# Kernel optimization log

Measured on AMD Instinct MI355X. Metric: run time of the kernel, lower is better.

The kernel has to match this reference:

```python
import jax, jax.numpy as jnp
import numpy as np

R = 3            # window radius -> (2R+1)^2 = 49 neighbors
N = 128          # grid side, n
K = 131          # 3 + 64 + 64 channels
C = 21           # num_classes
B = 2            # batch
W = (2 * R + 1) ** 2


def setup_inputs() -> dict:
    key = jax.random.key(0)
    k1, k2, k3, k4 = jax.random.split(key, 4)
    return {
        "intergrated": jax.random.normal(k1, (B, K, N, N), jnp.float32),
        "x2": jax.random.normal(k2, (B, C, N * N), jnp.float32),
        "sel_mask": jax.random.randint(k3, (B, N, N), 0, 2).astype(jnp.int32),
        "conv_parameter": jax.random.uniform(k4, (K,), jnp.float32),
    }


def _shifts(x, r):
    """Gather (2r+1)^2 shifted copies: x [..., n, n] -> [..., n, n, W].
    Entry w=(di,dj) holds x[i+di-r, j+dj-r] (zero-padded out of bounds)."""
    n = x.shape[-1]
    pad = [(0, 0)] * (x.ndim - 2) + [(r, r), (r, r)]
    xp = jnp.pad(x, pad)
    cols = [xp[..., di:di + n, dj:dj + n]
            for di in range(2 * r + 1) for dj in range(2 * r + 1)]
    return jnp.stack(cols, axis=-1)


def _rwn_single(feats, x2b, maskb, conv_parameter):
    """feats [K,n,n], x2b [C,n^2], maskb [n,n] int -> y [n^2, C]."""
    n = feats.shape[-1]
    m = maskb.astype(feats.dtype)            # sampled-pixel indicator
    xm = feats * m                            # sparse-sampled features [K,n,n]
    nbr = _shifts(xm, R)                      # [K,n,n,W] neighbor values
    valid = _shifts(jnp.ones((n, n), feats.dtype), R) > 0  # [n,n,W] in-bounds
    # per-channel windowed L1 distance, exp, per-pixel normalization (softmax
    # of +distance over the valid window, as in the original code)
    d = jnp.abs(xm[..., None] - nbr)          # [K,n,n,W]
    e = jnp.where(valid[None], jnp.exp(d), 0.0)
    a = e / e.sum(axis=-1, keepdims=True)     # rows sum to 1 per channel
    # W = sum_k conv_parameter[k] * a_k, rows only for selected pixels
    A = jnp.einsum('k,kijw->ijw', conv_parameter, a) * m[..., None]  # [n,n,W]
    # y[q,c] = sum_p W[p,q] * x2[p,c]  (W^T @ x2^T, per original col/row swap)
    feat = x2b.reshape(C, n, n)
    msg = A[None] * feat[..., None]           # [C,n,n,W]
    ypad = jnp.zeros((C, n + 2 * R, n + 2 * R), feats.dtype)
    w = 0
    for di in range(2 * R + 1):
        for dj in range(2 * R + 1):
            ypad = ypad.at[:, di:di + n, dj:dj + n].add(msg[..., w])
            w += 1
    y = ypad[:, R:R + n, R:R + n].reshape(C, n * n)
    return y.T                                 # [n^2, C]


def reference(intergrated, x2, sel_mask, conv_parameter):
    f = lambda fe, xb, mb: _rwn_single(fe, xb, mb, conv_parameter)
    return jax.vmap(f)(intergrated, x2, sel_mask)  # [B, n^2, C]
```

## Files before the change

### kernel.cpp

```cpp
#include <hip/hip_runtime.h>

#define R_ 3
#define D_ 7
#define W_ 49
#define N_ 128
#define K_ 131
#define C_ 21
#define B_ 2
#define NN (N_ * N_)
#define TI_ 8
#define TJ_ 16
#define PROWS (TI_ + 2 * R_)
#define PCOLS (TJ_ + 2 * R_)
#define PSTR 24
#define NELEM (PROWS * PCOLS)
#define LDSP (PROWS * PSTR + 8)
#define KC 8
#define KCHUNK ((K_ + KC - 1) / KC)
#define NTAP 28

__global__ __launch_bounds__(256) void rwn_affinity(
    const float* __restrict__ feats,
    const int*   __restrict__ mask,
    const float* __restrict__ cp,
    float* __restrict__ Aout)
{
    __shared__ float2 patch2[LDSP];

    const int tile = blockIdx.x;
    const int kc   = blockIdx.y;
    const int b    = blockIdx.z;
    const int tr = tile >> 3, tc = tile & 7;
    const int ti0 = tr * TI_, tj0 = tc * TJ_;

    const int tid = threadIdx.x;
    const int pix = tid >> 1;
    const int h   = tid & 1;
    const int ti = pix >> 4;
    const int tj = pix & 15;
    const int gi = ti0 + ti, gj = tj0 + tj;

    int   soff[2];
    float swt[2];
    float ozw[2];
    int   slds[2];
    #pragma unroll
    for (int r = 0; r < 2; ++r) {
        int e = tid + r * 256;
        bool act = (e < NELEM);
        int pr = e / PCOLS, pc = e - pr * PCOLS;
        int mi = ti0 + pr - R_, mj = tj0 + pc - R_;
        bool inb = act && mi >= 0 && mi < N_ && mj >= 0 && mj < N_;
        int cmi = mi < 0 ? 0 : (mi > N_ - 1 ? N_ - 1 : mi);
        int cmj = mj < 0 ? 0 : (mj > N_ - 1 ? N_ - 1 : mj);
        soff[r] = cmi * N_ + cmj;
        swt[r]  = inb ? (float)mask[b * NN + soff[r]] : 0.f;
        ozw[r]  = inb ? 1.f : 0.f;
        slds[r] = act ? (pr * PSTR + pc) : (PROWS * PSTR + 4);
    }

    const float ph = h ? 0.f : 1.f;
    const int cbase = ti * PSTR + tj;
    const int bh = cbase + h;

    float Aacc[NTAP];
    #pragma unroll
    for (int i = 0; i < NTAP; ++i) Aacc[i] = 0.f;

    const int k0 = kc * KCHUNK;
    const int k1 = (k0 + KCHUNK < K_) ? (k0 + KCHUNK) : K_;
    const float* fb = feats + (size_t)b * K_ * NN;

    for (int e = tid; e < LDSP; e += 256) patch2[e] = make_float2(0.f, 0.f);

    const float* fk0 = fb + (size_t)k0 * NN;
    float pre0 = fk0[soff[0]] * swt[0];
    float pre1 = fk0[soff[1]] * swt[1];

    __syncthreads();

    for (int k = k0; k < k1; ++k) {
        patch2[slds[0]] = make_float2(ozw[0] * __expf(pre0), ozw[0] * __expf(-pre0));
        patch2[slds[1]] = make_float2(ozw[1] * __expf(pre1), ozw[1] * __expf(-pre1));
        float n0 = 0.f, n1 = 0.f;
        if (k + 1 < k1) {
            const float* fn = fb + (size_t)(k + 1) * NN;
            n0 = fn[soff[0]] * swt[0];
            n1 = fn[soff[1]] * swt[1];
        }
        __syncthreads();

        const float2 cpair = patch2[cbase + R_ * PSTR + R_];
        float ex[NTAP];
        float dsum = 0.f;
        #pragma unroll
        for (int u = 0; u < D_; ++u) {
            #pragma unroll
            for (int s = 0; s < 4; ++s) {
                const int idx = u * 4 + s;
                const float2 np = patch2[bh + u * PSTR + 2 * s];
                float t = fmaxf(cpair.x * np.y, np.x * cpair.y);
                if (s == 3) t *= ph;
                ex[idx] = t;
                dsum += t;
            }
        }
        const float denom = dsum + __shfl_xor(dsum, 1, 64);
        const float scale = cp[k] * __frcp_rn(denom);
        #pragma unroll
        for (int idx = 0; idx < NTAP; ++idx) Aacc[idx] += scale * ex[idx];
        __syncthreads();

        pre0 = n0; pre1 = n1;
    }

    if (mask[b * NN + gi * N_ + gj] != 0) {
        const int pixg = gi * N_ + gj;
        float* ab = Aout + (size_t)b * W_ * NN + h * NN + pixg;
        #pragma unroll
        for (int u = 0; u < D_; ++u) {
            #pragma unroll
            for (int s = 0; s < 4; ++s) {
                if (h == 0 || s < 3)
                    atomicAdd(ab + (u * D_ + 2 * s) * NN, Aacc[u * 4 + s]);
            }
        }
    }
}

#define RSTR 25
__global__ __launch_bounds__(256) void rwn_gather(
    const float* __restrict__ Aarr,
    const float* __restrict__ x2,
    float* __restrict__ out)
{
    __shared__ float red[4 * 64 * RSTR];

    const int q0 = blockIdx.x * 64;
    const int b  = blockIdx.y;
    const int tid = threadIdx.x;
    const int qh = tid & 63;
    const int wg = tid >> 6;
    const int q = q0 + qh;
    const int i = q >> 7, j = q & (N_ - 1);

    const float* Ab = Aarr + (size_t)b * W_ * NN;
    const float* xb = x2 + (size_t)b * C_ * NN;

    float acc[C_];
    #pragma unroll
    for (int c = 0; c < C_; ++c) acc[c] = 0.f;

    #pragma unroll
    for (int rep = 0; rep < 2; ++rep) {
        const int uu = wg + rep * 4;
        if (uu > 6) break;
        const int pi = i - (uu - R_);
        const int cpi = pi < 0 ? 0 : (pi > N_ - 1 ? N_ - 1 : pi);
        const float rv = (pi >= 0 && pi < N_) ? 1.f : 0.f;
        const float* Aw = Ab + (size_t)uu * D_ * NN;
        #pragma unroll
        for (int v = 0; v < D_; ++v) {
            const int pj = j - (v - R_);
            const int cpj = pj < 0 ? 0 : (pj > N_ - 1 ? N_ - 1 : pj);
            const float vv = (pj >= 0 && pj < N_) ? rv : 0.f;
            const int p = cpi * N_ + cpj;
            const float a = vv * Aw[(size_t)v * NN + p];
            #pragma unroll
            for (int c = 0; c < C_; ++c)
                acc[c] += a * xb[(size_t)c * NN + p];
        }
    }

    float* rbase = red + (wg * 64 + qh) * RSTR;
    #pragma unroll
    for (int c = 0; c < C_; ++c) rbase[c] = acc[c];
    __syncthreads();

    float* ob = out + ((size_t)b * NN + q0) * C_;
    for (int e = tid; e < 64 * C_; e += 256) {
        const int qq = e / C_, cc = e - qq * C_;
        const int a = qq * RSTR + cc;
        ob[e] = red[a] + red[64 * RSTR + a] + red[128 * RSTR + a] + red[192 * RSTR + a];
    }
}

extern "C" void kernel_launch(void* const* d_in, const int* in_sizes, int n_in,
                              void* d_out, int out_size, void* d_ws, size_t ws_size,
                              hipStream_t stream) {
    const float* feats = (const float*)d_in[0];
    const float* x2    = (const float*)d_in[1];
    const int*   mask  = (const int*)d_in[2];
    const float* cp    = (const float*)d_in[3];
    float* out = (float*)d_out;

    float* Aarr = (float*)d_ws;
    const size_t Abytes = (size_t)B_ * W_ * NN * sizeof(float);

    hipMemsetAsync(Aarr, 0, Abytes, stream);

    dim3 gridA(128, KC, B_);
    rwn_affinity<<<gridA, 256, 0, stream>>>(feats, mask, cp, Aarr);

    dim3 gridG(NN / 64, B_);
    rwn_gather<<<gridG, 256, 0, stream>>>(Aarr, x2, out);
}
```

Measured before the change: 154.2 us.

## Use four threads per pixel and 512-thread blocks in affinity and gather

The affinity kernel now assigns four threads per pixel, each computing one or two full window rows (14 taps instead of 28), with a two-step shuffle reduction for the softmax denominator. The K split drops from 8 to 4 chunks, so there are fewer atomic adds per output element. The gather kernel uses 512 threads, giving one warp group per window row with an 8-way LDS reduction. The aim is more parallelism per pixel, lower register pressure and fewer redundant atomics, at the cost of a longer serial k-loop per block and more shuffle and LDS traffic.

```diff
diff --git a/kernel.cpp b/kernel.cpp
--- a/kernel.cpp
+++ b/kernel.cpp
@@ -14,12 +14,11 @@
 #define PCOLS (TJ_ + 2 * R_)
 #define PSTR 24
 #define NELEM (PROWS * PCOLS)
-#define LDSP (PROWS * PSTR + 8)
-#define KC 8
+#define LDSP ((PROWS + 1) * PSTR)
+#define KC 4
 #define KCHUNK ((K_ + KC - 1) / KC)
-#define NTAP 28
 
-__global__ __launch_bounds__(256) void rwn_affinity(
+__global__ __launch_bounds__(512, 4) void rwn_affinity(
     const float* __restrict__ feats,
     const int*   __restrict__ mask,
     const float* __restrict__ cp,
@@ -34,107 +33,98 @@
     const int ti0 = tr * TI_, tj0 = tc * TJ_;
 
     const int tid = threadIdx.x;
-    const int pix = tid >> 1;
-    const int h   = tid & 1;
+    const int pix = tid >> 2;
+    const int h   = tid & 3;
     const int ti = pix >> 4;
     const int tj = pix & 15;
     const int gi = ti0 + ti, gj = tj0 + tj;
 
-    int   soff[2];
-    float swt[2];
-    float ozw[2];
-    int   slds[2];
+    const bool act = (tid < NELEM);
+    int pr = tid / PCOLS, pc = tid - pr * PCOLS;
+    int mi = ti0 + pr - R_, mj = tj0 + pc - R_;
+    const bool inb = act && mi >= 0 && mi < N_ && mj >= 0 && mj < N_;
+    int cmi = mi < 0 ? 0 : (mi > N_ - 1 ? N_ - 1 : mi);
+    int cmj = mj < 0 ? 0 : (mj > N_ - 1 ? N_ - 1 : mj);
+    const int   soff = inb ? (cmi * N_ + cmj) : 0;
+    const float swt  = inb ? (float)mask[b * NN + soff] : 0.f;
+    const float ozw  = inb ? 1.f : 0.f;
+    const int   slds = pr * PSTR + pc;
+
+    const int cbase = ti * PSTR + tj;
+    const int ub0 = cbase + h * PSTR;
+    const int ub1 = (h < 3) ? (cbase + (h + 4) * PSTR) : (PROWS * PSTR + tj);
+
+    float Aacc[14];
     #pragma unroll
-    for (int r = 0; r < 2; ++r) {
-        int e = tid + r * 256;
-        bool act = (e < NELEM);
-        int pr = e / PCOLS, pc = e - pr * PCOLS;
-        int mi = ti0 + pr - R_, mj = tj0 + pc - R_;
-        bool inb = act && mi >= 0 && mi < N_ && mj >= 0 && mj < N_;
-        int cmi = mi < 0 ? 0 : (mi > N_ - 1 ? N_ - 1 : mi);
-        int cmj = mj < 0 ? 0 : (mj > N_ - 1 ? N_ - 1 : mj);
-        soff[r] = cmi * N_ + cmj;
-        swt[r]  = inb ? (float)mask[b * NN + soff[r]] : 0.f;
-        ozw[r]  = inb ? 1.f : 0.f;
-        slds[r] = act ? (pr * PSTR + pc) : (PROWS * PSTR + 4);
-    }
-
-    const float ph = h ? 0.f : 1.f;
-    const int cbase = ti * PSTR + tj;
-    const int bh = cbase + h;
-
-    float Aacc[NTAP];
-    #pragma unroll
-    for (int i = 0; i < NTAP; ++i) Aacc[i] = 0.f;
+    for (int i = 0; i < 14; ++i) Aacc[i] = 0.f;
 
     const int k0 = kc * KCHUNK;
     const int k1 = (k0 + KCHUNK < K_) ? (k0 + KCHUNK) : K_;
     const float* fb = feats + (size_t)b * K_ * NN;
 
-    for (int e = tid; e < LDSP; e += 256) patch2[e] = make_float2(0.f, 0.f);
+    for (int e = tid; e < PSTR; e += 512)
+        patch2[PROWS * PSTR + e] = make_float2(0.f, 0.f);
 
-    const float* fk0 = fb + (size_t)k0 * NN;
-    float pre0 = fk0[soff[0]] * swt[0];
-    float pre1 = fk0[soff[1]] * swt[1];
+    float pre = fb[(size_t)k0 * NN + soff] * swt;
 
     __syncthreads();
 
     for (int k = k0; k < k1; ++k) {
-        patch2[slds[0]] = make_float2(ozw[0] * __expf(pre0), ozw[0] * __expf(-pre0));
-        patch2[slds[1]] = make_float2(ozw[1] * __expf(pre1), ozw[1] * __expf(-pre1));
-        float n0 = 0.f, n1 = 0.f;
-        if (k + 1 < k1) {
-            const float* fn = fb + (size_t)(k + 1) * NN;
-            n0 = fn[soff[0]] * swt[0];
-            n1 = fn[soff[1]] * swt[1];
-        }
+        if (act)
+            patch2[slds] = make_float2(ozw * __expf(pre), ozw * __expf(-pre));
+        float nx = 0.f;
+        if (k + 1 < k1)
+            nx = fb[(size_t)(k + 1) * NN + soff] * swt;
         __syncthreads();
 
         const float2 cpair = patch2[cbase + R_ * PSTR + R_];
-        float ex[NTAP];
+        float ex[14];
         float dsum = 0.f;
         #pragma unroll
-        for (int u = 0; u < D_; ++u) {
-            #pragma unroll
-            for (int s = 0; s < 4; ++s) {
-                const int idx = u * 4 + s;
-                const float2 np = patch2[bh + u * PSTR + 2 * s];
-                float t = fmaxf(cpair.x * np.y, np.x * cpair.y);
-                if (s == 3) t *= ph;
-                ex[idx] = t;
-                dsum += t;
-            }
+        for (int v = 0; v < D_; ++v) {
+            const float2 np = patch2[ub0 + v];
+            float t = fmaxf(cpair.x * np.y, np.x * cpair.y);
+            ex[v] = t;
+            dsum += t;
         }
-        const float denom = dsum + __shfl_xor(dsum, 1, 64);
-        const float scale = cp[k] * __frcp_rn(denom);
         #pragma unroll
-        for (int idx = 0; idx < NTAP; ++idx) Aacc[idx] += scale * ex[idx];
+        for (int v = 0; v < D_; ++v) {
+            const float2 np = patch2[ub1 + v];
+            float t = fmaxf(cpair.x * np.y, np.x * cpair.y);
+            ex[7 + v] = t;
+            dsum += t;
+        }
+        dsum += __shfl_xor(dsum, 1, 64);
+        dsum += __shfl_xor(dsum, 2, 64);
+        const float scale = cp[k] * __frcp_rn(dsum);
+        #pragma unroll
+        for (int idx = 0; idx < 14; ++idx) Aacc[idx] += scale * ex[idx];
         __syncthreads();
 
-        pre0 = n0; pre1 = n1;
+        pre = nx;
     }
 
     if (mask[b * NN + gi * N_ + gj] != 0) {
         const int pixg = gi * N_ + gj;
-        float* ab = Aout + (size_t)b * W_ * NN + h * NN + pixg;
+        float* ab = Aout + (size_t)b * W_ * NN + pixg;
         #pragma unroll
-        for (int u = 0; u < D_; ++u) {
+        for (int v = 0; v < D_; ++v)
+            atomicAdd(ab + (h * D_ + v) * NN, Aacc[v]);
+        if (h < 3) {
             #pragma unroll
-            for (int s = 0; s < 4; ++s) {
-                if (h == 0 || s < 3)
-                    atomicAdd(ab + (u * D_ + 2 * s) * NN, Aacc[u * 4 + s]);
-            }
+            for (int v = 0; v < D_; ++v)
+                atomicAdd(ab + ((h + 4) * D_ + v) * NN, Aacc[7 + v]);
         }
     }
 }
 
-#define RSTR 25
-__global__ __launch_bounds__(256) void rwn_gather(
+#define RSTR 22
+__global__ __launch_bounds__(512, 4) void rwn_gather(
     const float* __restrict__ Aarr,
     const float* __restrict__ x2,
     float* __restrict__ out)
 {
-    __shared__ float red[4 * 64 * RSTR];
+    __shared__ float red[8 * 64 * RSTR];
 
     const int q0 = blockIdx.x * 64;
     const int b  = blockIdx.y;
@@ -151,14 +141,11 @@
     #pragma unroll
     for (int c = 0; c < C_; ++c) acc[c] = 0.f;
 
-    #pragma unroll
-    for (int rep = 0; rep < 2; ++rep) {
-        const int uu = wg + rep * 4;
-        if (uu > 6) break;
-        const int pi = i - (uu - R_);
+    if (wg < D_) {
+        const int pi = i - (wg - R_);
         const int cpi = pi < 0 ? 0 : (pi > N_ - 1 ? N_ - 1 : pi);
         const float rv = (pi >= 0 && pi < N_) ? 1.f : 0.f;
-        const float* Aw = Ab + (size_t)uu * D_ * NN;
+        const float* Aw = Ab + (size_t)wg * D_ * NN;
         #pragma unroll
         for (int v = 0; v < D_; ++v) {
             const int pj = j - (v - R_);
@@ -178,10 +165,14 @@
     __syncthreads();
 
     float* ob = out + ((size_t)b * NN + q0) * C_;
-    for (int e = tid; e < 64 * C_; e += 256) {
+    for (int e = tid; e < 64 * C_; e += 512) {
         const int qq = e / C_, cc = e - qq * C_;
         const int a = qq * RSTR + cc;
-        ob[e] = red[a] + red[64 * RSTR + a] + red[128 * RSTR + a] + red[192 * RSTR + a];
+        float s = 0.f;
+        #pragma unroll
+        for (int pl = 0; pl < 8; ++pl)
+            s += red[pl * 64 * RSTR + a];
+        ob[e] = s;
     }
 }
 
@@ -200,8 +191,8 @@
     hipMemsetAsync(Aarr, 0, Abytes, stream);
 
     dim3 gridA(128, KC, B_);
-    rwn_affinity<<<gridA, 256, 0, stream>>>(feats, mask, cp, Aarr);
+    rwn_affinity<<<gridA, 512, 0, stream>>>(feats, mask, cp, Aarr);
 
     dim3 gridG(NN / 64, B_);
-    rwn_gather<<<gridG, 256, 0, stream>>>(Aarr, x2, out);
+    rwn_gather<<<gridG, 512, 0, stream>>>(Aarr, x2, out);
 }
```

Measured after the change: 164.9 us. +6.9%, slower.

## Accumulate affinity taps in packed fp16 and widen gather to one row per wave

Applied to the files above, without the earlier changes.

The affinity kernel now packs pairs of window taps into half-precision vectors and does the per-channel scale-and-accumulate with packed fp16 FMAs. This halves the accumulator register count and the FMA instruction count. The exponentials switch to exp2f, with log2(e) folded into the mask weight. The gather kernel goes from 256 to 512 threads so that each of 7 waves handles one window row, and its final reduction sums 8 partial planes. The fp16 accumulation costs accuracy and can overflow when channel distances are large.

```diff
diff --git a/kernel.cpp b/kernel.cpp
--- a/kernel.cpp
+++ b/kernel.cpp
@@ -1,4 +1,5 @@
 #include <hip/hip_runtime.h>
+#include <hip/hip_fp16.h>
 
 #define R_ 3
 #define D_ 7
@@ -17,7 +18,8 @@
 #define LDSP (PROWS * PSTR + 8)
 #define KC 8
 #define KCHUNK ((K_ + KC - 1) / KC)
-#define NTAP 28
+
+typedef __fp16 h2 __attribute__((ext_vector_type(2)));
 
 __global__ __launch_bounds__(256) void rwn_affinity(
     const float* __restrict__ feats,
@@ -40,6 +42,7 @@
     const int tj = pix & 15;
     const int gi = ti0 + ti, gj = tj0 + tj;
 
+    const float LOG2E = 1.4426950408889634f;
     int   soff[2];
     float swt[2];
     float ozw[2];
@@ -54,7 +57,7 @@
         int cmi = mi < 0 ? 0 : (mi > N_ - 1 ? N_ - 1 : mi);
         int cmj = mj < 0 ? 0 : (mj > N_ - 1 ? N_ - 1 : mj);
         soff[r] = cmi * N_ + cmj;
-        swt[r]  = inb ? (float)mask[b * NN + soff[r]] : 0.f;
+        swt[r]  = inb ? ((float)mask[b * NN + soff[r]] * LOG2E) : 0.f;
         ozw[r]  = inb ? 1.f : 0.f;
         slds[r] = act ? (pr * PSTR + pc) : (PROWS * PSTR + 4);
     }
@@ -63,9 +66,9 @@
     const int cbase = ti * PSTR + tj;
     const int bh = cbase + h;
 
-    float Aacc[NTAP];
-    #pragma unroll
-    for (int i = 0; i < NTAP; ++i) Aacc[i] = 0.f;
+    h2 Aacc[14];
+    #pragma unroll
+    for (int i = 0; i < 14; ++i) Aacc[i] = (h2){(__fp16)0.f, (__fp16)0.f};
 
     const int k0 = kc * KCHUNK;
     const int k1 = (k0 + KCHUNK < K_) ? (k0 + KCHUNK) : K_;
@@ -80,8 +83,8 @@
     __syncthreads();
 
     for (int k = k0; k < k1; ++k) {
-        patch2[slds[0]] = make_float2(ozw[0] * __expf(pre0), ozw[0] * __expf(-pre0));
-        patch2[slds[1]] = make_float2(ozw[1] * __expf(pre1), ozw[1] * __expf(-pre1));
+        patch2[slds[0]] = make_float2(ozw[0] * exp2f(pre0), ozw[0] * exp2f(-pre0));
+        patch2[slds[1]] = make_float2(ozw[1] * exp2f(pre1), ozw[1] * exp2f(-pre1));
         float n0 = 0.f, n1 = 0.f;
         if (k + 1 < k1) {
             const float* fn = fb + (size_t)(k + 1) * NN;
@@ -91,24 +94,27 @@
         __syncthreads();
 
         const float2 cpair = patch2[cbase + R_ * PSTR + R_];
-        float ex[NTAP];
+        h2 ex[14];
         float dsum = 0.f;
         #pragma unroll
         for (int u = 0; u < D_; ++u) {
             #pragma unroll
-            for (int s = 0; s < 4; ++s) {
-                const int idx = u * 4 + s;
-                const float2 np = patch2[bh + u * PSTR + 2 * s];
-                float t = fmaxf(cpair.x * np.y, np.x * cpair.y);
-                if (s == 3) t *= ph;
-                ex[idx] = t;
-                dsum += t;
+            for (int m = 0; m < 2; ++m) {
+                const float2 np0 = patch2[bh + u * PSTR + 4 * m];
+                const float2 np1 = patch2[bh + u * PSTR + 4 * m + 2];
+                float t0 = fmaxf(cpair.x * np0.y, np0.x * cpair.y);
+                float t1 = fmaxf(cpair.x * np1.y, np1.x * cpair.y);
+                if (m == 1) t1 *= ph;
+                dsum += t0;
+                dsum += t1;
+                ex[u * 2 + m] = __builtin_amdgcn_cvt_pkrtz(t0, t1);
             }
         }
         const float denom = dsum + __shfl_xor(dsum, 1, 64);
         const float scale = cp[k] * __frcp_rn(denom);
-        #pragma unroll
-        for (int idx = 0; idx < NTAP; ++idx) Aacc[idx] += scale * ex[idx];
+        const h2 s2 = __builtin_amdgcn_cvt_pkrtz(scale, scale);
+        #pragma unroll
+        for (int m = 0; m < 14; ++m) Aacc[m] = ex[m] * s2 + Aacc[m];
         __syncthreads();
 
         pre0 = n0; pre1 = n1;
@@ -120,21 +126,23 @@
         #pragma unroll
         for (int u = 0; u < D_; ++u) {
             #pragma unroll
-            for (int s = 0; s < 4; ++s) {
-                if (h == 0 || s < 3)
-                    atomicAdd(ab + (u * D_ + 2 * s) * NN, Aacc[u * 4 + s]);
+            for (int m = 0; m < 2; ++m) {
+                const h2 tv = Aacc[u * 2 + m];
+                atomicAdd(ab + (u * D_ + 4 * m) * NN, (float)tv[0]);
+                if (h == 0 || m < 1)
+                    atomicAdd(ab + (u * D_ + 4 * m + 2) * NN, (float)tv[1]);
             }
         }
     }
 }
 
-#define RSTR 25
-__global__ __launch_bounds__(256) void rwn_gather(
+#define RSTR 22
+__global__ __launch_bounds__(512, 4) void rwn_gather(
     const float* __restrict__ Aarr,
     const float* __restrict__ x2,
     float* __restrict__ out)
 {
-    __shared__ float red[4 * 64 * RSTR];
+    __shared__ float red[8 * 64 * RSTR];
 
     const int q0 = blockIdx.x * 64;
     const int b  = blockIdx.y;
@@ -151,14 +159,11 @@
     #pragma unroll
     for (int c = 0; c < C_; ++c) acc[c] = 0.f;
 
-    #pragma unroll
-    for (int rep = 0; rep < 2; ++rep) {
-        const int uu = wg + rep * 4;
-        if (uu > 6) break;
-        const int pi = i - (uu - R_);
+    if (wg < D_) {
+        const int pi = i - (wg - R_);
         const int cpi = pi < 0 ? 0 : (pi > N_ - 1 ? N_ - 1 : pi);
         const float rv = (pi >= 0 && pi < N_) ? 1.f : 0.f;
-        const float* Aw = Ab + (size_t)uu * D_ * NN;
+        const float* Aw = Ab + (size_t)wg * D_ * NN;
         #pragma unroll
         for (int v = 0; v < D_; ++v) {
             const int pj = j - (v - R_);
@@ -178,10 +183,14 @@
     __syncthreads();
 
     float* ob = out + ((size_t)b * NN + q0) * C_;
-    for (int e = tid; e < 64 * C_; e += 256) {
+    for (int e = tid; e < 64 * C_; e += 512) {
         const int qq = e / C_, cc = e - qq * C_;
         const int a = qq * RSTR + cc;
-        ob[e] = red[a] + red[64 * RSTR + a] + red[128 * RSTR + a] + red[192 * RSTR + a];
+        float s = 0.f;
+        #pragma unroll
+        for (int pl = 0; pl < 8; ++pl)
+            s += red[pl * 64 * RSTR + a];
+        ob[e] = s;
     }
 }
 
@@ -197,11 +206,11 @@
     float* Aarr = (float*)d_ws;
     const size_t Abytes = (size_t)B_ * W_ * NN * sizeof(float);
 
-    hipMemsetAsync(Aarr, 0, Abytes, stream);
+    (void)hipMemsetAsync(Aarr, 0, Abytes, stream);
 
     dim3 gridA(128, KC, B_);
     rwn_affinity<<<gridA, 256, 0, stream>>>(feats, mask, cp, Aarr);
 
     dim3 gridG(NN / 64, B_);
-    rwn_gather<<<gridG, 256, 0, stream>>>(Aarr, x2, out);
+    rwn_gather<<<gridG, 512, 0, stream>>>(Aarr, x2, out);
 }
```

Result: faster. 149.9 us (-2.8%).
